# Optimization experiments

Hardware: AMD Instinct MI355X
Metric: run time of the kernel (lower is better)

Reference implementation:

```python
import jax, jax.numpy as jnp
import numpy as np

TEMPERATURE = 30.0


def _adaptive_pool_28(sk):
    # sk: [b, 1, H, W] with H, W divisible by 28 -> [b, 1, 28, 28]
    b, c, h, w = sk.shape
    fh, fw = h // 28, w // 28
    return sk.reshape(b, c, 28, fh, 28, fw).mean(axis=(3, 5))


def setup_inputs() -> dict:
    key = jax.random.key(0)
    ks = jax.random.split(key, 6)
    bs, C, H, W, K = 8, 256, 64, 64, 16
    return {
        "x": jax.random.normal(ks[0], (bs, C, H, W), dtype=jnp.float32),
        "scene_knowledge": jax.random.normal(ks[1], (bs, 1, 56, 56), dtype=jnp.float32),
        "weight": jax.random.normal(ks[2], (K, C, C, 3, 3), dtype=jnp.float32) * 0.02,
        "bias": jax.random.normal(ks[3], (K, C), dtype=jnp.float32) * 0.02,
        "att_w1": jax.random.normal(ks[4], (196, 784), dtype=jnp.float32) * 0.05,
        "att_w2": jax.random.normal(ks[5], (16, 196), dtype=jnp.float32) * 0.05,
    }


def reference(x, scene_knowledge, weight, bias, att_w1, att_w2):
    bs, C, h, w = x.shape
    K = weight.shape[0]

    # ---- Attention: pooled scene knowledge -> softmax over K experts ----
    pooled = _adaptive_pool_28(scene_knowledge).reshape(bs, 28 * 28)  # [bs, 784]
    hdn = jax.nn.relu(pooled @ att_w1.T)                               # [bs, 196]
    logits = hdn @ att_w2.T                                            # [bs, K]
    att = jax.nn.softmax(logits / TEMPERATURE, axis=-1)                # [bs, K]

    # ---- Aggregate per-sample conv weights and biases ----
    agg_w = jnp.einsum("bk,koihw->boihw", att, weight)  # [bs, C, C, 3, 3]
    agg_b = att @ bias                                   # [bs, C]

    # ---- Per-sample conv (equivalent to groups=bs trick in torch) ----
    def per_sample_conv(xi, wi):
        # xi: [C, h, w], wi: [C, C, 3, 3]
        return jax.lax.conv_general_dilated(
            xi[None], wi, window_strides=(1, 1), padding="SAME",
            dimension_numbers=("NCHW", "OIHW", "NCHW"))[0]

    out = jax.vmap(per_sample_conv)(x, agg_w)            # [bs, C, h, w]
    out = out + agg_b[:, :, None, None] + x              # bias + residual
    return out
```

## Files before the change

kernel.cpp:

```cpp
#include <hip/hip_runtime.h>
#include <stdint.h>
#include <stddef.h>

typedef __bf16 bf16;
typedef __bf16 bf16x8 __attribute__((ext_vector_type(8)));
typedef __bf16 bf16x4 __attribute__((ext_vector_type(4)));
typedef float f32x4 __attribute__((ext_vector_type(4)));

static_assert(sizeof(bf16x8) == 16, "bf16x8 must be 16B");

__device__ __forceinline__ void gload_lds16(const void* g, void* l) {
    __builtin_amdgcn_global_load_lds(
        (const __attribute__((address_space(1))) uint32_t*)g,
        (__attribute__((address_space(3))) uint32_t*)l, 16, 0, 0);
}

__global__ void prep_kernel(const float* __restrict__ x, bf16* __restrict__ xt,
                            const float* __restrict__ sk,
                            const float* __restrict__ w1,
                            const float* __restrict__ w2,
                            float* __restrict__ att) {
    __shared__ bf16 T[256 * 64];
    __shared__ float pooled[784];
    __shared__ float hdn[196];
    __shared__ float logits[16];
    const int t = threadIdx.x;

    if (blockIdx.x < 512) {
        const int bid = blockIdx.x;
        const int b = bid >> 6, y = bid & 63;
        const float* src = x + (size_t)b * 256 * 4096 + (size_t)y * 64;
        for (int i = 0; i < 16; ++i) {
            int v = t + 256 * i;
            int ci = v >> 4, x4 = (v & 15) * 4;
            float4 f = *(const float4*)(src + (size_t)ci * 4096 + x4);
            bf16* d = &T[ci * 64 + x4];
            d[0] = (bf16)f.x; d[1] = (bf16)f.y; d[2] = (bf16)f.z; d[3] = (bf16)f.w;
        }
        __syncthreads();
        bf16* dstb = xt + (size_t)bid * 16384;
        for (int i = 0; i < 8; ++i) {
            int c2 = t + 256 * i;
            int cg = c2 >> 6, xx = c2 & 63;
            bf16x8 v;
#pragma unroll
            for (int c = 0; c < 8; ++c) v[c] = T[(cg * 8 + c) * 64 + xx];
            *(bf16x8*)(dstb + (size_t)c2 * 8) = v;
        }
    } else {
        const int b = blockIdx.x - 512;
        const float* skb = sk + (size_t)b * 3136;
        for (int e = t; e < 784; e += 256) {
            int oy = e / 28, ox = e % 28;
            const float* p = skb + (oy * 2) * 56 + ox * 2;
            pooled[e] = 0.25f * (p[0] + p[1] + p[56] + p[57]);
        }
        __syncthreads();
        if (t < 196) {
            float s = 0.f;
            const float* wr = w1 + (size_t)t * 784;
            for (int i = 0; i < 784; ++i) s += pooled[i] * wr[i];
            hdn[t] = s > 0.f ? s : 0.f;
        }
        __syncthreads();
        if (t < 16) {
            float s = 0.f;
            const float* wr = w2 + (size_t)t * 196;
            for (int j = 0; j < 196; ++j) s += hdn[j] * wr[j];
            logits[t] = s * (1.0f / 30.0f);
        }
        __syncthreads();
        if (t == 0) {
            float m = logits[0];
            for (int k = 1; k < 16; ++k) m = fmaxf(m, logits[k]);
            float e16[16], sum = 0.f;
            for (int k = 0; k < 16; ++k) { e16[k] = expf(logits[k] - m); sum += e16[k]; }
            float inv = 1.f / sum;
            for (int k = 0; k < 16; ++k) att[b * 16 + k] = e16[k] * inv;
        }
    }
}

__global__ __launch_bounds__(256) void agg_kernel(
    const float* __restrict__ weight,
    const float* __restrict__ bias,
    const float* __restrict__ att,
    bf16* __restrict__ aggw,
    float* __restrict__ aggb) {
    const int bid = blockIdx.x;
    const int co = bid & 255, chunk = bid >> 8;
    const int t = threadIdx.x;

    __shared__ bf16 accW[8 * 576];

    if (chunk == 0 && t < 8) {
        float s = 0.f;
        for (int k = 0; k < 16; ++k) s += att[t * 16 + k] * bias[k * 256 + co];
        aggb[t * 256 + co] = s;
    }

    if (t < 144) {
        const float* wbase = weight + (size_t)co * 2304 + (size_t)chunk * 576 + (size_t)t * 4;
        float4 wv[16];
#pragma unroll
        for (int k = 0; k < 16; ++k)
            wv[k] = *(const float4*)(wbase + (size_t)k * 589824);
        float a[8][4];
#pragma unroll
        for (int b = 0; b < 8; ++b)
#pragma unroll
            for (int j = 0; j < 4; ++j) a[b][j] = 0.f;
#pragma unroll
        for (int k = 0; k < 16; ++k) {
#pragma unroll
            for (int b = 0; b < 8; ++b) {
                const float av = att[b * 16 + k];
                a[b][0] += av * wv[k].x;
                a[b][1] += av * wv[k].y;
                a[b][2] += av * wv[k].z;
                a[b][3] += av * wv[k].w;
            }
        }
#pragma unroll
        for (int b = 0; b < 8; ++b) {
            bf16x4 v;
#pragma unroll
            for (int j = 0; j < 4; ++j) v[j] = (bf16)a[b][j];
            *(bf16x4*)&accW[b * 576 + t * 4] = v;
        }
    }
    __syncthreads();

    const int half = co >> 7, co_l = co & 127;
    for (int s = t; s < 576; s += 256) {
        const int b = s / 72, r = s - b * 72;
        const int pos = r >> 3, cg = r & 7;
        bf16x8 v;
#pragma unroll
        for (int c = 0; c < 8; ++c) v[c] = accW[b * 576 + (cg * 8 + c) * 9 + pos];
        size_t o = (((((size_t)b * 9 + pos) * 4 + chunk) * 2 + half) * 8 + cg) * 128 + co_l;
        *(bf16x8*)(aggw + o * 8) = v;
    }
}

__global__ __launch_bounds__(256, 2) void conv_kernel(
    const bf16* __restrict__ xt, const bf16* __restrict__ aggw,
    const float* __restrict__ aggb, const float* __restrict__ xin,
    float* __restrict__ out) {
    const int bid = blockIdx.x;
    const int ytile = bid & 31;
    const int half = (bid >> 5) & 1;
    const int b = bid >> 6;
    const int tid = threadIdx.x;
    const int wave = tid >> 6, lane = tid & 63;
    const int wm = wave & 1, wn = wave >> 1;
    const int lane15 = lane & 15, quad = lane >> 4;

    __shared__ __align__(16) bf16 Xs[4][8][66][8];
    __shared__ __align__(16) bf16 Ws[2][8][128][8];

    f32x4 acc[4][4];
#pragma unroll
    for (int mt = 0; mt < 4; ++mt)
#pragma unroll
        for (int nt = 0; nt < 4; ++nt) acc[mt][nt] = f32x4{0.f, 0.f, 0.f, 0.f};

    {
        uint4 z; z.x = z.y = z.z = z.w = 0u;
        uint4* p = (uint4*)&Xs[0][0][0][0];
        for (int i = tid; i < 2112; i += 256) p[i] = z;
    }
    __syncthreads();

    const int yrow = ytile * 2 - 1 + wave;
    const bool rowok = (yrow >= 0) && (yrow < 64);
    const bf16* xsrc = xt + ((size_t)b * 64 + (rowok ? yrow : 0)) * 16384 + (size_t)lane * 8;
    bf16* xdstbase = &Xs[wave][0][1][0];

    auto stageX = [&](int chunk) {
        if (rowok) {
            const bf16* s0 = xsrc + (size_t)chunk * 4096;
#pragma unroll
            for (int cg = 0; cg < 8; ++cg)
                gload_lds16(s0 + cg * 512, xdstbase + cg * 528);
        }
    };
    auto loadW = [&](int chunk, int pos, int buf) {
        const bf16* wsrc = aggw + ((((size_t)b * 9 + pos) * 4 + chunk) * 2 + half) * 8192
                           + wave * 2048 + (size_t)lane * 8;
        bf16* wdst = ((bf16*)Ws) + (size_t)buf * 8192 + wave * 2048;
#pragma unroll
        for (int i = 0; i < 4; ++i)
            gload_lds16(wsrc + i * 512, wdst + i * 512);
    };

    stageX(0);
    loadW(0, 0, 0);
    __syncthreads();

    for (int chunk = 0; chunk < 4; ++chunk) {
#pragma unroll
        for (int pos = 0; pos < 9; ++pos) {
            const int par = (chunk + pos) & 1;
            const bool last = (chunk == 3) && (pos == 8);
            if (!last) {
                const int nc = (pos == 8) ? chunk + 1 : chunk;
                const int np = (pos == 8) ? 0 : pos + 1;
                loadW(nc, np, par ^ 1);
            }
            const int kh = pos / 3, kw = pos - kh * 3;
            const int xr = wn + kh;
#pragma unroll
            for (int s = 0; s < 2; ++s) {
                const int cg = s * 4 + quad;
                bf16x8 afr[4], bfr[4];
#pragma unroll
                for (int mt = 0; mt < 4; ++mt)
                    afr[mt] = *(const bf16x8*)&Ws[par][cg][wm * 64 + mt * 16 + lane15][0];
#pragma unroll
                for (int nt = 0; nt < 4; ++nt)
                    bfr[nt] = *(const bf16x8*)&Xs[xr][cg][kw + nt * 16 + lane15][0];
#pragma unroll
                for (int mt = 0; mt < 4; ++mt)
#pragma unroll
                    for (int nt = 0; nt < 4; ++nt)
                        acc[mt][nt] = __builtin_amdgcn_mfma_f32_16x16x32_bf16(
                            afr[mt], bfr[nt], acc[mt][nt], 0, 0, 0);
            }
            if (!last) {
                __syncthreads();
                if (pos == 8) {
                    stageX(chunk + 1);
                    __syncthreads();
                }
            }
        }
    }

    const int y = ytile * 2 + wn;
#pragma unroll
    for (int mt = 0; mt < 4; ++mt) {
#pragma unroll
        for (int r = 0; r < 4; ++r) {
            const int co = half * 128 + wm * 64 + mt * 16 + quad * 4 + r;
            const float bbv = aggb[b * 256 + co];
            const size_t rowbase = (((size_t)b * 256 + co) * 64 + y) * 64;
#pragma unroll
            for (int nt = 0; nt < 4; ++nt) {
                const size_t oidx = rowbase + nt * 16 + lane15;
                out[oidx] = acc[mt][nt][r] + bbv + xin[oidx];
            }
        }
    }
}

extern "C" void kernel_launch(void* const* d_in, const int* in_sizes, int n_in,
                              void* d_out, int out_size, void* d_ws, size_t ws_size,
                              hipStream_t stream) {
    const float* x    = (const float*)d_in[0];
    const float* sk   = (const float*)d_in[1];
    const float* wgt  = (const float*)d_in[2];
    const float* bias = (const float*)d_in[3];
    const float* w1   = (const float*)d_in[4];
    const float* w2   = (const float*)d_in[5];
    float* out = (float*)d_out;

    char* ws = (char*)d_ws;
    float* att  = (float*)(ws + 0);
    float* aggb = (float*)(ws + 1024);
    bf16*  aggw = (bf16*)(ws + 16384);
    bf16*  xt   = (bf16*)(ws + 16384 + 9437184);

    prep_kernel<<<520, 256, 0, stream>>>(x, xt, sk, w1, w2, att);
    agg_kernel<<<1024, 256, 0, stream>>>(wgt, bias, att, aggw, aggb);
    conv_kernel<<<512, 256, 0, stream>>>(xt, aggw, aggb, x, out);
}
```

Measured before the change: 203.3 us.

## Load conv weights directly to registers and double-buffer input tile in LDS

The conv kernel no longer stages the aggregated weights through LDS. Each wave loads its A fragments straight from global memory into a double-buffered register array, prefetching the next tap. The input row tile is now double-buffered in LDS and prefetched one channel chunk ahead, which cuts per-tap barriers to one per chunk. This trades LDS traffic and syncs for more registers and uncoalesced per-lane global weight reads. The attention MLP in the prep kernel also switches to wave-parallel dot products with shuffle reductions.

```diff
diff --git a/kernel.cpp b/kernel.cpp
--- a/kernel.cpp
+++ b/kernel.cpp
@@ -49,6 +49,7 @@
         }
     } else {
         const int b = blockIdx.x - 512;
+        const int wave = t >> 6, lane = t & 63;
         const float* skb = sk + (size_t)b * 3136;
         for (int e = t; e < 784; e += 256) {
             int oy = e / 28, ox = e % 28;
@@ -56,18 +57,22 @@
             pooled[e] = 0.25f * (p[0] + p[1] + p[56] + p[57]);
         }
         __syncthreads();
-        if (t < 196) {
+        for (int j = wave; j < 196; j += 4) {
+            const float* wr = w1 + (size_t)j * 784;
             float s = 0.f;
-            const float* wr = w1 + (size_t)t * 784;
-            for (int i = 0; i < 784; ++i) s += pooled[i] * wr[i];
-            hdn[t] = s > 0.f ? s : 0.f;
-        }
-        __syncthreads();
-        if (t < 16) {
+            for (int i = lane; i < 784; i += 64) s += pooled[i] * wr[i];
+#pragma unroll
+            for (int off = 32; off; off >>= 1) s += __shfl_down(s, off, 64);
+            if (lane == 0) hdn[j] = s > 0.f ? s : 0.f;
+        }
+        __syncthreads();
+        for (int j = wave; j < 16; j += 4) {
+            const float* wr = w2 + (size_t)j * 196;
             float s = 0.f;
-            const float* wr = w2 + (size_t)t * 196;
-            for (int j = 0; j < 196; ++j) s += hdn[j] * wr[j];
-            logits[t] = s * (1.0f / 30.0f);
+            for (int i = lane; i < 196; i += 64) s += hdn[i] * wr[i];
+#pragma unroll
+            for (int off = 32; off; off >>= 1) s += __shfl_down(s, off, 64);
+            if (lane == 0) logits[j] = s * (1.0f / 30.0f);
         }
         __syncthreads();
         if (t == 0) {
@@ -156,8 +161,7 @@
     const int wm = wave & 1, wn = wave >> 1;
     const int lane15 = lane & 15, quad = lane >> 4;
 
-    __shared__ __align__(16) bf16 Xs[4][8][66][8];
-    __shared__ __align__(16) bf16 Ws[2][8][128][8];
+    __shared__ __align__(16) bf16 Xs[2][4][8][66][8];
 
     f32x4 acc[4][4];
 #pragma unroll
@@ -167,74 +171,69 @@
 
     {
         uint4 z; z.x = z.y = z.z = z.w = 0u;
-        uint4* p = (uint4*)&Xs[0][0][0][0];
-        for (int i = tid; i < 2112; i += 256) p[i] = z;
-    }
-    __syncthreads();
+        uint4* p = (uint4*)&Xs[0][0][0][0][0];
+        for (int i = tid; i < 4224; i += 256) p[i] = z;
+    }
 
     const int yrow = ytile * 2 - 1 + wave;
     const bool rowok = (yrow >= 0) && (yrow < 64);
     const bf16* xsrc = xt + ((size_t)b * 64 + (rowok ? yrow : 0)) * 16384 + (size_t)lane * 8;
-    bf16* xdstbase = &Xs[wave][0][1][0];
-
-    auto stageX = [&](int chunk) {
+
+    auto stageX = [&](int chunk, int buf) {
         if (rowok) {
             const bf16* s0 = xsrc + (size_t)chunk * 4096;
+            bf16* d0 = &Xs[buf][wave][0][1][0];
 #pragma unroll
             for (int cg = 0; cg < 8; ++cg)
-                gload_lds16(s0 + cg * 512, xdstbase + cg * 528);
+                gload_lds16(s0 + cg * 512, d0 + cg * 528);
         }
     };
-    auto loadW = [&](int chunk, int pos, int buf) {
-        const bf16* wsrc = aggw + ((((size_t)b * 9 + pos) * 4 + chunk) * 2 + half) * 8192
-                           + wave * 2048 + (size_t)lane * 8;
-        bf16* wdst = ((bf16*)Ws) + (size_t)buf * 8192 + wave * 2048;
-#pragma unroll
-        for (int i = 0; i < 4; ++i)
-            gload_lds16(wsrc + i * 512, wdst + i * 512);
+
+    bf16x8 afr[2][8];
+    auto loadA = [&](int par, int chunk, int pos) {
+        const bf16* ab = aggw + ((((size_t)b * 9 + pos) * 4 + chunk) * 2 + half) * 8192;
+#pragma unroll
+        for (int s = 0; s < 2; ++s)
+#pragma unroll
+            for (int mt = 0; mt < 4; ++mt)
+                afr[par][s * 4 + mt] = *(const bf16x8*)(
+                    ab + (size_t)((s * 4 + quad) * 128 + wm * 64 + mt * 16 + lane15) * 8);
     };
 
-    stageX(0);
-    loadW(0, 0, 0);
     __syncthreads();
+    stageX(0, 0);
+    loadA(0, 0, 0);
+    __syncthreads();
 
     for (int chunk = 0; chunk < 4; ++chunk) {
+        const int xb = chunk & 1;
 #pragma unroll
         for (int pos = 0; pos < 9; ++pos) {
             const int par = (chunk + pos) & 1;
-            const bool last = (chunk == 3) && (pos == 8);
-            if (!last) {
+            if (!(chunk == 3 && pos == 8)) {
                 const int nc = (pos == 8) ? chunk + 1 : chunk;
                 const int np = (pos == 8) ? 0 : pos + 1;
-                loadW(nc, np, par ^ 1);
-            }
+                loadA(par ^ 1, nc, np);
+            }
+            if (pos == 0 && chunk < 3) stageX(chunk + 1, xb ^ 1);
             const int kh = pos / 3, kw = pos - kh * 3;
             const int xr = wn + kh;
 #pragma unroll
             for (int s = 0; s < 2; ++s) {
                 const int cg = s * 4 + quad;
-                bf16x8 afr[4], bfr[4];
-#pragma unroll
-                for (int mt = 0; mt < 4; ++mt)
-                    afr[mt] = *(const bf16x8*)&Ws[par][cg][wm * 64 + mt * 16 + lane15][0];
+                bf16x8 bfr[4];
 #pragma unroll
                 for (int nt = 0; nt < 4; ++nt)
-                    bfr[nt] = *(const bf16x8*)&Xs[xr][cg][kw + nt * 16 + lane15][0];
+                    bfr[nt] = *(const bf16x8*)&Xs[xb][xr][cg][kw + nt * 16 + lane15][0];
 #pragma unroll
                 for (int mt = 0; mt < 4; ++mt)
 #pragma unroll
                     for (int nt = 0; nt < 4; ++nt)
                         acc[mt][nt] = __builtin_amdgcn_mfma_f32_16x16x32_bf16(
-                            afr[mt], bfr[nt], acc[mt][nt], 0, 0, 0);
-            }
-            if (!last) {
-                __syncthreads();
-                if (pos == 8) {
-                    stageX(chunk + 1);
-                    __syncthreads();
-                }
-            }
-        }
+                            afr[par][s * 4 + mt], bfr[nt], acc[mt][nt], 0, 0, 0);
+            }
+        }
+        if (chunk < 3) __syncthreads();
     }
 
     const int y = ytile * 2 + wn;
```

New measurement: 361.1 us. 1.78x slower.
